# Kernel optimization log

Measured on AMD Instinct MI355X. Metric: run time of the kernel, lower is better.

The kernel has to match this reference:

```python
import jax, jax.numpy as jnp
import numpy as np

N_NODES = 100000
N_EDGES = 3200000
D = 256


def setup_inputs() -> dict:
    key = jax.random.key(0)
    ks = jax.random.split(key, 8)
    ego_embeddings = jax.random.normal(ks[0], (N_NODES, D), dtype=jnp.float32) * 0.1
    edge_vals = jax.random.uniform(ks[1], (N_EDGES,), dtype=jnp.float32) / 32.0  # ~normalized adjacency
    W1 = jax.random.normal(ks[2], (D, D), dtype=jnp.float32) * (1.0 / np.sqrt(D))
    b1 = jnp.zeros((D,), dtype=jnp.float32)
    W2 = jax.random.normal(ks[3], (D, D), dtype=jnp.float32) * (1.0 / np.sqrt(D))
    b2 = jnp.zeros((D,), dtype=jnp.float32)
    edge_rows = jax.random.randint(ks[4], (N_EDGES,), 0, N_NODES, dtype=jnp.int32)
    edge_cols = jax.random.randint(ks[5], (N_EDGES,), 0, N_NODES, dtype=jnp.int32)
    return {"ego_embeddings": ego_embeddings, "edge_vals": edge_vals,
            "W1": W1, "b1": b1, "W2": W2, "b2": b2,
            "edge_rows": edge_rows, "edge_cols": edge_cols}


def reference(ego_embeddings, edge_vals, W1, b1, W2, b2, edge_rows, edge_cols):
    # SpMM: side = A_in @ ego  (A_in in COO: rows, cols, vals)
    n = ego_embeddings.shape[0]
    gathered = ego_embeddings[edge_cols] * edge_vals[:, None]      # [E, D]
    side = jax.ops.segment_sum(gathered, edge_rows, num_segments=n)  # [N, D]
    # bi-interaction aggregator
    sum_emb = jax.nn.leaky_relu((ego_embeddings + side) @ W1.T + b1, negative_slope=0.01)
    bi_emb = jax.nn.leaky_relu((ego_embeddings * side) @ W2.T + b2, negative_slope=0.01)
    # dropout p=0.0 -> identity
    return sum_emb + bi_emb
```

## Files before the change

### kernel.cpp

```cpp
#include <hip/hip_runtime.h>
#include <hip/hip_fp16.h>
#include <stdint.h>

#define D 256
#define CHSH 13
#define NPW 25

typedef __attribute__((ext_vector_type(8))) short short8;
typedef __attribute__((ext_vector_type(4))) float floatx4;

__device__ __forceinline__ ushort f2bf(float f) {
    union { float f; uint32_t u; } v; v.f = f;
    uint32_t u = v.u;
    u += 0x7fffu + ((u >> 16) & 1u);
    return (ushort)(u >> 16);
}
__device__ __forceinline__ float bf2f(ushort h) {
    union { uint32_t u; float f; } v; v.u = ((uint32_t)h) << 16;
    return v.f;
}


__global__ void k_hist(const int* __restrict__ er, const int* __restrict__ ec,
                       const float* __restrict__ ev,
                       int* __restrict__ bp, uint64_t* __restrict__ aux,
                       int E, int n) {
    int e = blockIdx.x * 256 + threadIdx.x;
    if (e >= E) return;
    int row = er[e];
    int col = ec[e];
    int b = (col >> CHSH) * n + row;
    atomicAdd(&bp[b], 1);
    ushort hb = __half_as_ushort(__float2half_rn(ev[e]));
    uint32_t payload = ((uint32_t)col << 15) | (uint32_t)hb;
    aux[e] = ((uint64_t)(uint32_t)b << 32) | payload;
}

__global__ void k_red(const int* __restrict__ bp, int* __restrict__ part, int nb) {
    __shared__ int s[256];
    int t = threadIdx.x;
    int base = blockIdx.x * 1024 + t * 4;
    int v = 0;
#pragma unroll
    for (int j = 0; j < 4; ++j) if (base + j < nb) v += (bp[base + j] + 3) & ~3;
    s[t] = v; __syncthreads();
    for (int off = 128; off; off >>= 1) {
        if (t < off) s[t] += s[t + off];
        __syncthreads();
    }
    if (t == 0) part[blockIdx.x] = s[0];
}

__global__ __launch_bounds__(1024) void k_scanpart(int* __restrict__ part, int np) {
    __shared__ int s[1024];
    int t = threadIdx.x;
    int p0 = (2 * t < np) ? part[2 * t] : 0;
    int p1 = (2 * t + 1 < np) ? part[2 * t + 1] : 0;
    int v = p0 + p1;
    s[t] = v; __syncthreads();
    for (int off = 1; off < 1024; off <<= 1) {
        int x = (t >= off) ? s[t - off] : 0;
        __syncthreads();
        s[t] += x;
        __syncthreads();
    }
    int excl = s[t] - v;
    if (2 * t < np) part[2 * t] = excl;
    if (2 * t + 1 < np) part[2 * t + 1] = excl + p0;
}

__global__ void k_scan3(int* __restrict__ bp, int* __restrict__ bp2,
                        const int* __restrict__ part, int nb) {
    __shared__ int s[256];
    int t = threadIdx.x;
    int base = blockIdx.x * 1024 + t * 4;
    int p0 = 0, p1 = 0, p2 = 0, p3 = 0;
    if (base     < nb) p0 = (bp[base]     + 3) & ~3;
    if (base + 1 < nb) p1 = (bp[base + 1] + 3) & ~3;
    if (base + 2 < nb) p2 = (bp[base + 2] + 3) & ~3;
    if (base + 3 < nb) p3 = (bp[base + 3] + 3) & ~3;
    int sum = p0 + p1 + p2 + p3;
    s[t] = sum; __syncthreads();
    for (int off = 1; off < 256; off <<= 1) {
        int x = (t >= off) ? s[t - off] : 0;
        __syncthreads();
        s[t] += x;
        __syncthreads();
    }
    int run = part[blockIdx.x] + s[t] - sum;
    if (base     < nb) { bp[base]     = run; bp2[base]     = run; if (base     == nb - 1) bp2[nb] = run + p0; } run += p0;
    if (base + 1 < nb) { bp[base + 1] = run; bp2[base + 1] = run; if (base + 1 == nb - 1) bp2[nb] = run + p1; } run += p1;
    if (base + 2 < nb) { bp[base + 2] = run; bp2[base + 2] = run; if (base + 2 == nb - 1) bp2[nb] = run + p2; } run += p2;
    if (base + 3 < nb) { bp[base + 3] = run; bp2[base + 3] = run; if (base + 3 == nb - 1) bp2[nb] = run + p3; }
}

__global__ void k_scatter(const uint64_t* __restrict__ aux,
                          int* __restrict__ bp, uint32_t* __restrict__ csr,
                          int E, int BW) {
    int xcd = blockIdx.x & 7;
    int j = blockIdx.x >> 3;
    int e = j * 256 + threadIdx.x;
    if (e >= E) return;
    uint64_t a = aux[e];
    int b = (int)(a >> 32);
    int lo = xcd * BW;
    if (b < lo || b >= lo + BW) return;
    int p = atomicAdd(&bp[b], 1);
    csr[p] = (uint32_t)a;
}

__global__ void k_cvt(const float4* __restrict__ ego, ushort4* __restrict__ ego_bf,
                      const float4* __restrict__ W1, const float4* __restrict__ W2,
                      ushort4* __restrict__ W1b, ushort4* __restrict__ W2b, int n4) {
    int i = blockIdx.x * 256 + threadIdx.x;
    const float4* src;
    ushort4* dst;
    if (i < n4) { src = ego + i; dst = ego_bf + i; }
    else {
        int j = i - n4;
        if (j >= 32768) return;
        int k = j & 16383;
        src = ((j < 16384) ? W1 : W2) + k;
        dst = ((j < 16384) ? W1b : W2b) + k;
    }
    float4 f = *src;
    ushort4 u;
    u.x = f2bf(f.x); u.y = f2bf(f.y); u.z = f2bf(f.z); u.w = f2bf(f.w);
    *dst = u;
}

__global__ __launch_bounds__(256, 4) void k_spmm(
        const ushort* __restrict__ ego_bf, const int* __restrict__ bp2,
        const uint32_t* __restrict__ csr,
        ushort* __restrict__ X1, ushort* __restrict__ X2, int n, int NCH, int nb) {
    int wid = __builtin_amdgcn_readfirstlane(blockIdx.x * 4 + (threadIdx.x >> 6));
    int lane = threadIdx.x & 63;
    int node0 = wid * NPW;
    if (node0 >= n) return;
    int d0 = lane * 4;

    float acc[NPW][4];
#pragma unroll
    for (int i = 0; i < NPW; ++i) {
        acc[i][0] = 0.f; acc[i][1] = 0.f; acc[i][2] = 0.f; acc[i][3] = 0.f;
    }

    for (int c = 0; c < NCH; ++c) {
        int B[NPW + 1];
#pragma unroll
        for (int i = 0; i <= NPW; ++i) {
            int idx = c * n + node0 + i;
            B[i] = bp2[idx > nb ? nb : idx];
        }
#pragma unroll
        for (int i = 0; i < NPW; ++i) {
            if (node0 + i < n) {
                int end = B[i + 1];
                for (int e = B[i]; e < end; e += 4) {
                    uint32_t w0 = csr[e], w1 = csr[e + 1], w2 = csr[e + 2], w3 = csr[e + 3];
                    ushort4 u0 = *(const ushort4*)(ego_bf + (size_t)(w0 >> 15) * D + d0);
                    ushort4 u1 = *(const ushort4*)(ego_bf + (size_t)(w1 >> 15) * D + d0);
                    ushort4 u2 = *(const ushort4*)(ego_bf + (size_t)(w2 >> 15) * D + d0);
                    ushort4 u3 = *(const ushort4*)(ego_bf + (size_t)(w3 >> 15) * D + d0);
                    float v0 = __half2float(__ushort_as_half((ushort)(w0 & 0x7fff)));
                    float v1 = __half2float(__ushort_as_half((ushort)(w1 & 0x7fff)));
                    float v2 = __half2float(__ushort_as_half((ushort)(w2 & 0x7fff)));
                    float v3 = __half2float(__ushort_as_half((ushort)(w3 & 0x7fff)));
                    acc[i][0] += v0 * bf2f(u0.x); acc[i][1] += v0 * bf2f(u0.y);
                    acc[i][2] += v0 * bf2f(u0.z); acc[i][3] += v0 * bf2f(u0.w);
                    acc[i][0] += v1 * bf2f(u1.x); acc[i][1] += v1 * bf2f(u1.y);
                    acc[i][2] += v1 * bf2f(u1.z); acc[i][3] += v1 * bf2f(u1.w);
                    acc[i][0] += v2 * bf2f(u2.x); acc[i][1] += v2 * bf2f(u2.y);
                    acc[i][2] += v2 * bf2f(u2.z); acc[i][3] += v2 * bf2f(u2.w);
                    acc[i][0] += v3 * bf2f(u3.x); acc[i][1] += v3 * bf2f(u3.y);
                    acc[i][2] += v3 * bf2f(u3.z); acc[i][3] += v3 * bf2f(u3.w);
                }
            }
        }
    }

#pragma unroll
    for (int i = 0; i < NPW; ++i) {
        int node = node0 + i;
        if (node < n) {
            ushort4 eg = *(const ushort4*)(ego_bf + (size_t)node * D + d0);
            float e0 = bf2f(eg.x), e1 = bf2f(eg.y), e2 = bf2f(eg.z), e3 = bf2f(eg.w);
            ushort4 o1, o2;
            o1.x = f2bf(e0 + acc[i][0]); o2.x = f2bf(e0 * acc[i][0]);
            o1.y = f2bf(e1 + acc[i][1]); o2.y = f2bf(e1 * acc[i][1]);
            o1.z = f2bf(e2 + acc[i][2]); o2.z = f2bf(e2 * acc[i][2]);
            o1.w = f2bf(e3 + acc[i][3]); o2.w = f2bf(e3 * acc[i][3]);
            *(ushort4*)(X1 + (size_t)node * D + d0) = o1;
            *(ushort4*)(X2 + (size_t)node * D + d0) = o2;
        }
    }
}

__global__ __launch_bounds__(256) void k_gemm(
        const ushort* __restrict__ X1, const ushort* __restrict__ X2,
        const ushort* __restrict__ W1b, const ushort* __restrict__ W2b,
        const float* __restrict__ b1, const float* __restrict__ b2,
        float* __restrict__ out, int n) {
    int lane = threadIdx.x & 63;
    int w = threadIdx.x >> 6;
    int l16 = lane & 15, quad = lane >> 4;
    int row0 = blockIdx.x * 64;
    int colw = w * 64;

    floatx4 acc1[4][4], acc2[4][4];
#pragma unroll
    for (int i = 0; i < 4; ++i)
#pragma unroll
        for (int j = 0; j < 4; ++j) { acc1[i][j] = (floatx4)0.f; acc2[i][j] = (floatx4)0.f; }

    for (int kk = 0; kk < D; kk += 32) {
        short8 a[4], b[4];
#pragma unroll
        for (int mt = 0; mt < 4; ++mt)
            a[mt] = *(const short8*)(X1 + (size_t)(row0 + mt * 16 + l16) * D + kk + quad * 8);
#pragma unroll
        for (int nt = 0; nt < 4; ++nt)
            b[nt] = *(const short8*)(W1b + (size_t)(colw + nt * 16 + l16) * D + kk + quad * 8);
#pragma unroll
        for (int mt = 0; mt < 4; ++mt)
#pragma unroll
            for (int nt = 0; nt < 4; ++nt)
                acc1[mt][nt] = __builtin_amdgcn_mfma_f32_16x16x32_bf16(a[mt], b[nt], acc1[mt][nt], 0, 0, 0);
    }
    for (int kk = 0; kk < D; kk += 32) {
        short8 a[4], b[4];
#pragma unroll
        for (int mt = 0; mt < 4; ++mt)
            a[mt] = *(const short8*)(X2 + (size_t)(row0 + mt * 16 + l16) * D + kk + quad * 8);
#pragma unroll
        for (int nt = 0; nt < 4; ++nt)
            b[nt] = *(const short8*)(W2b + (size_t)(colw + nt * 16 + l16) * D + kk + quad * 8);
#pragma unroll
        for (int mt = 0; mt < 4; ++mt)
#pragma unroll
            for (int nt = 0; nt < 4; ++nt)
                acc2[mt][nt] = __builtin_amdgcn_mfma_f32_16x16x32_bf16(a[mt], b[nt], acc2[mt][nt], 0, 0, 0);
    }

#pragma unroll
    for (int nt = 0; nt < 4; ++nt) {
        int col = colw + nt * 16 + l16;
        float bb1 = b1[col], bb2 = b2[col];
#pragma unroll
        for (int mt = 0; mt < 4; ++mt) {
            int row = row0 + mt * 16 + quad * 4;
#pragma unroll
            for (int r = 0; r < 4; ++r) {
                if (row + r < n) {
                    float v1 = acc1[mt][nt][r] + bb1;
                    v1 = v1 > 0.f ? v1 : 0.01f * v1;
                    float v2 = acc2[mt][nt][r] + bb2;
                    v2 = v2 > 0.f ? v2 : 0.01f * v2;
                    out[(size_t)(row + r) * D + col] = v1 + v2;
                }
            }
        }
    }
}

extern "C" void kernel_launch(void* const* d_in, const int* in_sizes, int n_in,
                              void* d_out, int out_size, void* d_ws, size_t ws_size,
                              hipStream_t stream) {
    const float* ego   = (const float*)d_in[0];
    const float* evals = (const float*)d_in[1];
    const float* W1    = (const float*)d_in[2];
    const float* b1    = (const float*)d_in[3];
    const float* W2    = (const float*)d_in[4];
    const float* b2    = (const float*)d_in[5];
    const int* erows   = (const int*)d_in[6];
    const int* ecols   = (const int*)d_in[7];
    float* out = (float*)d_out;

    int n = in_sizes[0] / D;
    int E = in_sizes[1];
    int npad = (n + 63) & ~63;
    int NCH = (n + (1 << CHSH) - 1) >> CHSH;
    int nb = n * NCH;
    int np = (nb + 1023) / 1024;
    int BW = (nb + 7) / 8;
    size_t csr_cap = (size_t)E + 3u * (size_t)nb;

    char* p = (char*)d_ws;
    auto alloc = [&](size_t bytes) {
        char* q = p;
        p += (bytes + 511) & ~(size_t)511;
        return q;
    };
    ushort* ego_bf = (ushort*)alloc((size_t)n * D * 2);
    ushort* X1     = (ushort*)alloc((size_t)npad * D * 2);
    ushort* X2     = (ushort*)alloc((size_t)npad * D * 2);
    ushort* W1b    = (ushort*)alloc((size_t)D * D * 2);
    ushort* W2b    = (ushort*)alloc((size_t)D * D * 2);
    int* bp        = (int*)alloc((size_t)nb * 4);
    int* bp2       = (int*)alloc((size_t)(nb + 64) * 4);
    int* part      = (int*)alloc((size_t)np * 4);
    uint32_t* csr  = (uint32_t*)alloc(csr_cap * 4);

    uint64_t* aux = (uint64_t*)X1;

    hipMemsetAsync(bp, 0, (size_t)nb * 4, stream);
    hipMemsetAsync(csr, 0, csr_cap * 4, stream);
    int EB = (E + 255) / 256;
    k_hist<<<EB, 256, 0, stream>>>(erows, ecols, evals, bp, aux, E, n);
    k_red<<<np, 256, 0, stream>>>(bp, part, nb);
    k_scanpart<<<1, 1024, 0, stream>>>(part, np);
    k_scan3<<<np, 256, 0, stream>>>(bp, bp2, part, nb);
    k_scatter<<<8 * EB, 256, 0, stream>>>(aux, bp, csr, E, BW);

    int n4 = n * (D / 4);
    k_cvt<<<(n4 + 32768 + 255) / 256, 256, 0, stream>>>((const float4*)ego, (ushort4*)ego_bf,
                                                        (const float4*)W1, (const float4*)W2,
                                                        (ushort4*)W1b, (ushort4*)W2b, n4);

    int nwaves = (n + NPW - 1) / NPW;
    int nblocks = (nwaves + 3) / 4;
    k_spmm<<<nblocks, 256, 0, stream>>>(ego_bf, bp2, csr, X1, X2, n, NCH, nb);

    k_gemm<<<npad / 64, 256, 0, stream>>>(X1, X2, W1b, W2b, b1, b2, out, n);
}
```

Baseline: 867.6 us.

## Guarantee one padded edge group per bucket and issue first groups unconditionally

Every (chunk,row) bucket in the CSR is now padded to at least four entries, so each row has at least one group of four edges. For full warps, the SpMM kernel issues the first group of all 25 rows without loop bounds checks, which exposes many independent gathers at once for memory-level parallelism, and then handles the remaining groups. Launch bounds drop from 4 to 3 blocks per SM to leave room for the extra live registers. The cost is extra padding entries and wasted gathers for empty buckets (13 chunks per node), a larger CSR, and lower occupancy.

```diff
diff --git a/kernel.cpp b/kernel.cpp
--- a/kernel.cpp
+++ b/kernel.cpp
@@ -18,6 +18,10 @@
 __device__ __forceinline__ float bf2f(ushort h) {
     union { uint32_t u; float f; } v; v.u = ((uint32_t)h) << 16;
     return v.f;
+}
+
+__device__ __forceinline__ int pad4(int x) {
+    return ((x + 3) & ~3) + ((x == 0) ? 4 : 0);
 }
 
 
@@ -42,7 +46,7 @@
     int base = blockIdx.x * 1024 + t * 4;
     int v = 0;
 #pragma unroll
-    for (int j = 0; j < 4; ++j) if (base + j < nb) v += (bp[base + j] + 3) & ~3;
+    for (int j = 0; j < 4; ++j) if (base + j < nb) v += pad4(bp[base + j]);
     s[t] = v; __syncthreads();
     for (int off = 128; off; off >>= 1) {
         if (t < off) s[t] += s[t + off];
@@ -75,10 +79,10 @@
     int t = threadIdx.x;
     int base = blockIdx.x * 1024 + t * 4;
     int p0 = 0, p1 = 0, p2 = 0, p3 = 0;
-    if (base     < nb) p0 = (bp[base]     + 3) & ~3;
-    if (base + 1 < nb) p1 = (bp[base + 1] + 3) & ~3;
-    if (base + 2 < nb) p2 = (bp[base + 2] + 3) & ~3;
-    if (base + 3 < nb) p3 = (bp[base + 3] + 3) & ~3;
+    if (base     < nb) p0 = pad4(bp[base]);
+    if (base + 1 < nb) p1 = pad4(bp[base + 1]);
+    if (base + 2 < nb) p2 = pad4(bp[base + 2]);
+    if (base + 3 < nb) p3 = pad4(bp[base + 3]);
     int sum = p0 + p1 + p2 + p3;
     s[t] = sum; __syncthreads();
     for (int off = 1; off < 256; off <<= 1) {
@@ -129,7 +133,28 @@
     *dst = u;
 }
 
-__global__ __launch_bounds__(256, 4) void k_spmm(
+#define GROUP(ii, ee) do {                                                    \
+    int e_ = (ee);                                                            \
+    uint32_t w0 = csr[e_], w1 = csr[e_ + 1], w2 = csr[e_ + 2], w3 = csr[e_ + 3]; \
+    ushort4 u0 = *(const ushort4*)(ego_bf + (size_t)(w0 >> 15) * D + d0);     \
+    ushort4 u1 = *(const ushort4*)(ego_bf + (size_t)(w1 >> 15) * D + d0);     \
+    ushort4 u2 = *(const ushort4*)(ego_bf + (size_t)(w2 >> 15) * D + d0);     \
+    ushort4 u3 = *(const ushort4*)(ego_bf + (size_t)(w3 >> 15) * D + d0);     \
+    float v0 = __half2float(__ushort_as_half((ushort)(w0 & 0x7fff)));         \
+    float v1 = __half2float(__ushort_as_half((ushort)(w1 & 0x7fff)));         \
+    float v2 = __half2float(__ushort_as_half((ushort)(w2 & 0x7fff)));         \
+    float v3 = __half2float(__ushort_as_half((ushort)(w3 & 0x7fff)));         \
+    acc[ii][0] += v0 * bf2f(u0.x); acc[ii][1] += v0 * bf2f(u0.y);             \
+    acc[ii][2] += v0 * bf2f(u0.z); acc[ii][3] += v0 * bf2f(u0.w);             \
+    acc[ii][0] += v1 * bf2f(u1.x); acc[ii][1] += v1 * bf2f(u1.y);             \
+    acc[ii][2] += v1 * bf2f(u1.z); acc[ii][3] += v1 * bf2f(u1.w);             \
+    acc[ii][0] += v2 * bf2f(u2.x); acc[ii][1] += v2 * bf2f(u2.y);             \
+    acc[ii][2] += v2 * bf2f(u2.z); acc[ii][3] += v2 * bf2f(u2.w);             \
+    acc[ii][0] += v3 * bf2f(u3.x); acc[ii][1] += v3 * bf2f(u3.y);             \
+    acc[ii][2] += v3 * bf2f(u3.z); acc[ii][3] += v3 * bf2f(u3.w);             \
+} while (0)
+
+__global__ __launch_bounds__(256, 3) void k_spmm(
         const ushort* __restrict__ ego_bf, const int* __restrict__ bp2,
         const uint32_t* __restrict__ csr,
         ushort* __restrict__ X1, ushort* __restrict__ X2, int n, int NCH, int nb) {
@@ -145,6 +170,7 @@
         acc[i][0] = 0.f; acc[i][1] = 0.f; acc[i][2] = 0.f; acc[i][3] = 0.f;
     }
 
+    bool full = (node0 + NPW <= n);
     for (int c = 0; c < NCH; ++c) {
         int B[NPW + 1];
 #pragma unroll
@@ -152,30 +178,17 @@
             int idx = c * n + node0 + i;
             B[i] = bp2[idx > nb ? nb : idx];
         }
-#pragma unroll
-        for (int i = 0; i < NPW; ++i) {
-            if (node0 + i < n) {
-                int end = B[i + 1];
-                for (int e = B[i]; e < end; e += 4) {
-                    uint32_t w0 = csr[e], w1 = csr[e + 1], w2 = csr[e + 2], w3 = csr[e + 3];
-                    ushort4 u0 = *(const ushort4*)(ego_bf + (size_t)(w0 >> 15) * D + d0);
-                    ushort4 u1 = *(const ushort4*)(ego_bf + (size_t)(w1 >> 15) * D + d0);
-                    ushort4 u2 = *(const ushort4*)(ego_bf + (size_t)(w2 >> 15) * D + d0);
-                    ushort4 u3 = *(const ushort4*)(ego_bf + (size_t)(w3 >> 15) * D + d0);
-                    float v0 = __half2float(__ushort_as_half((ushort)(w0 & 0x7fff)));
-                    float v1 = __half2float(__ushort_as_half((ushort)(w1 & 0x7fff)));
-                    float v2 = __half2float(__ushort_as_half((ushort)(w2 & 0x7fff)));
-                    float v3 = __half2float(__ushort_as_half((ushort)(w3 & 0x7fff)));
-                    acc[i][0] += v0 * bf2f(u0.x); acc[i][1] += v0 * bf2f(u0.y);
-                    acc[i][2] += v0 * bf2f(u0.z); acc[i][3] += v0 * bf2f(u0.w);
-                    acc[i][0] += v1 * bf2f(u1.x); acc[i][1] += v1 * bf2f(u1.y);
-                    acc[i][2] += v1 * bf2f(u1.z); acc[i][3] += v1 * bf2f(u1.w);
-                    acc[i][0] += v2 * bf2f(u2.x); acc[i][1] += v2 * bf2f(u2.y);
-                    acc[i][2] += v2 * bf2f(u2.z); acc[i][3] += v2 * bf2f(u2.w);
-                    acc[i][0] += v3 * bf2f(u3.x); acc[i][1] += v3 * bf2f(u3.y);
-                    acc[i][2] += v3 * bf2f(u3.z); acc[i][3] += v3 * bf2f(u3.w);
-                }
-            }
+        if (full) {
+#pragma unroll
+            for (int i = 0; i < NPW; ++i) GROUP(i, B[i]);
+#pragma unroll
+            for (int i = 0; i < NPW; ++i)
+                for (int e = B[i] + 4; e < B[i + 1]; e += 4) GROUP(i, e);
+        } else {
+#pragma unroll
+            for (int i = 0; i < NPW; ++i)
+                if (node0 + i < n)
+                    for (int e = B[i]; e < B[i + 1]; e += 4) GROUP(i, e);
         }
     }
 
@@ -283,7 +296,7 @@
     int nb = n * NCH;
     int np = (nb + 1023) / 1024;
     int BW = (nb + 7) / 8;
-    size_t csr_cap = (size_t)E + 3u * (size_t)nb;
+    size_t csr_cap = (size_t)E + 4u * (size_t)nb;
 
     char* p = (char*)d_ws;
     auto alloc = [&](size_t bytes) {
```

Measured after the change: 1.815 ms. +109.2%, slower.
